# Kernel tuning notes

Hardware: AMD Instinct MI355X
Metric: run time of the kernel (lower is better)

The kernel has to match this reference:

```python
import jax, jax.numpy as jnp
import numpy as np

SEQ_LEN, BATCH, HID, ATT = 2048, 64, 512, 512


def setup_inputs() -> dict:
    key = jax.random.key(0)
    k1, k2, k3, k4, k5, k6 = jax.random.split(key, 6)
    return {
        "dec_out": jax.random.normal(k1, (BATCH, HID), dtype=jnp.float32),
        "enc_outs": jax.random.normal(k2, (SEQ_LEN, BATCH, HID), dtype=jnp.float32),
        "W_s": jax.random.normal(k3, (ATT, HID), dtype=jnp.float32) * (1.0 / np.sqrt(HID)),
        "W_t": jax.random.normal(k4, (ATT, HID), dtype=jnp.float32) * (1.0 / np.sqrt(HID)),
        "b_t": jax.random.normal(k5, (ATT,), dtype=jnp.float32) * 0.01,
        "v_a": jax.random.uniform(k6, (ATT,), dtype=jnp.float32, minval=-0.05, maxval=0.05),
    }


def reference(dec_out, enc_outs, W_s, W_t, b_t, v_a):
    # enc_att: (seq_len, batch, att) = W_s @ enc_outs
    enc_att = jnp.einsum('sbh,ah->sba', enc_outs, W_s)
    # dec_att: (batch, att) = W_t @ dec_out + b_t
    dec_att = dec_out @ W_t.T + b_t
    # score(b, s) = v_a . tanh(enc_att[s,b] + dec_att[b])
    scores = jnp.einsum('sba,a->bs', jnp.tanh(enc_att + dec_att[None, :, :]), v_a)
    return scores  # (batch, seq_len)
```

## Files before the change

kernel.cpp:

```cpp
#include <hip/hip_runtime.h>

typedef __attribute__((ext_vector_type(8))) short short8;
typedef __attribute__((ext_vector_type(4))) float f32x4;

#define SEQ 2048
#define BATCH 64
#define HID 512
#define ATT 512

__device__ __forceinline__ unsigned short f2bf(float f) {
  unsigned u = __float_as_uint(f);
  u += 0x7fffu + ((u >> 16) & 1u);
  return (unsigned short)(u >> 16);
}

__device__ __forceinline__ void dma16(const void* g, void* l) {
  __builtin_amdgcn_global_load_lds(
      (const __attribute__((address_space(1))) unsigned int*)g,
      (__attribute__((address_space(3))) unsigned int*)l, 16, 0, 0);
}

__device__ __forceinline__ short8 cvt8(float4 lo, float4 hi) {
  union { unsigned u[4]; short8 s; } r;
  asm("v_cvt_pk_bf16_f32 %0, %1, %2" : "=v"(r.u[0]) : "v"(lo.x), "v"(lo.y));
  asm("v_cvt_pk_bf16_f32 %0, %1, %2" : "=v"(r.u[1]) : "v"(lo.z), "v"(lo.w));
  asm("v_cvt_pk_bf16_f32 %0, %1, %2" : "=v"(r.u[2]) : "v"(hi.x), "v"(hi.y));
  asm("v_cvt_pk_bf16_f32 %0, %1, %2" : "=v"(r.u[3]) : "v"(hi.z), "v"(hi.w));
  return r.s;
}

#define GLOADS(dst, voff, base, OFF) \
  asm volatile("global_load_dwordx4 %0, %1, %2 offset:" #OFF \
               : "=v"(dst) : "v"(voff), "s"(base))

#define BWAIT(N, b0, b1, b2, b3) \
  asm volatile("s_waitcnt vmcnt(" #N ")" \
               : "+v"(b0), "+v"(b1), "+v"(b2), "+v"(b3) :: "memory")

__global__ void bahdanau_pre(const float* __restrict__ dec_out,
                             const float* __restrict__ W_t,
                             const float* __restrict__ b_t,
                             const float* __restrict__ W_s,
                             unsigned short* __restrict__ wsb,
                             float* __restrict__ decT) {
  if (blockIdx.x < 64) {
    const int b = blockIdx.x;
    __shared__ float drow[HID];
    for (int i = threadIdx.x; i < HID; i += 256) drow[i] = dec_out[b * HID + i];
    __syncthreads();
    for (int a = threadIdx.x; a < ATT; a += 256) {
      const float4* wr = (const float4*)(W_t + (size_t)a * HID);
      float s0 = 0.f, s1 = 0.f, s2 = 0.f, s3 = 0.f;
#pragma unroll 4
      for (int j = 0; j < HID / 4; ++j) {
        float4 w = wr[j];
        s0 = fmaf(w.x, drow[4 * j + 0], s0);
        s1 = fmaf(w.y, drow[4 * j + 1], s1);
        s2 = fmaf(w.z, drow[4 * j + 2], s2);
        s3 = fmaf(w.w, drow[4 * j + 3], s3);
      }
      decT[a * BATCH + b] = (s0 + s1) + (s2 + s3) + b_t[a];
    }
  } else {
    const int cb = blockIdx.x - 64;
    const float4* src = (const float4*)W_s;
#pragma unroll
    for (int i = 0; i < 4; ++i) {
      int idx = cb * 1024 + i * 256 + threadIdx.x;
      float4 v = src[idx];
      int a = idx >> 7;
      int h = (idx & 127) * 4;
      ushort4 o;
      o.x = f2bf(v.x); o.y = f2bf(v.y); o.z = f2bf(v.z); o.w = f2bf(v.w);
      int blk = (a >> 4) * 64 + ((h >> 3) & 3) * 16 + (a & 15);
      int dst = (h >> 5) * 16384 + blk * 8 + (h & 7);
      *(ushort4*)&wsb[dst] = o;
    }
  }
}

__global__ __launch_bounds__(512, 4)
void bahdanau_main(const float* __restrict__ enc,
                   const unsigned short* __restrict__ wsb,
                   const float* __restrict__ decT,
                   const float* __restrict__ v_a,
                   float* __restrict__ out) {
  __shared__ __align__(16) float Asm[4][2048];
  __shared__ float partial[512];

  const int tid  = threadIdx.x;
  const int w    = tid >> 6;
  const int lane = tid & 63;
  const int c = lane & 15;
  const int q = lane >> 4;
  const int s = blockIdx.x;
  const int n0 = w * 64;

  const char* encB = (const char*)(enc + (size_t)s * 64 * HID);

  const int am = (w & 3) * 16 + c;
  const int ag = q * 2 + (w >> 2);
  const char* aSrc = encB + am * 2048 + ag * 16;

  const unsigned voff = (unsigned)(w * 256 + q * 16 + c) * 16u;

  f32x4 acc[4][4];
#pragma unroll
  for (int nt = 0; nt < 4; ++nt)
#pragma unroll
    for (int mt = 0; mt < 4; ++mt)
      acc[mt][nt] = *(const f32x4*)(decT + (size_t)(n0 + nt * 16 + c) * 64 + mt * 16 + q * 4);

  asm volatile("s_waitcnt vmcnt(0)" ::: "memory");

  short8 bf[2][4];

  dma16(aSrc, &Asm[0][w * 256]);
  GLOADS(bf[0][0], voff, wsb, 0);
  GLOADS(bf[0][1], voff, wsb, 1024);
  GLOADS(bf[0][2], voff, wsb, 2048);
  GLOADS(bf[0][3], voff, wsb, 3072);
  dma16(aSrc + 128, &Asm[1][w * 256]);

#pragma unroll
  for (int kb = 0; kb < 16; ++kb) {
    if (kb + 1 < 16) {
      const unsigned short* bk = wsb + (size_t)(kb + 1) * 16384;
      GLOADS(bf[(kb + 1) & 1][0], voff, bk, 0);
      GLOADS(bf[(kb + 1) & 1][1], voff, bk, 1024);
      GLOADS(bf[(kb + 1) & 1][2], voff, bk, 2048);
      GLOADS(bf[(kb + 1) & 1][3], voff, bk, 3072);
    }
    if (kb + 2 < 16)
      dma16(aSrc + (kb + 2) * 128, &Asm[(kb + 2) & 3][w * 256]);

    if (kb <= 13)      BWAIT(6, bf[kb & 1][0], bf[kb & 1][1], bf[kb & 1][2], bf[kb & 1][3]);
    else if (kb == 14) BWAIT(5, bf[kb & 1][0], bf[kb & 1][1], bf[kb & 1][2], bf[kb & 1][3]);
    else               BWAIT(0, bf[kb & 1][0], bf[kb & 1][1], bf[kb & 1][2], bf[kb & 1][3]);
    __builtin_amdgcn_s_barrier();

    const float* Ac = &Asm[kb & 3][0];
#pragma unroll
    for (int mt = 0; mt < 4; ++mt) {
      float4 lo = *(const float4*)(Ac + (mt * 64 + q * 16 + c) * 4);
      float4 hi = *(const float4*)(Ac + (256 + mt * 64 + q * 16 + c) * 4);
      short8 af = cvt8(lo, hi);
#pragma unroll
      for (int nt = 0; nt < 4; ++nt)
        acc[mt][nt] = __builtin_amdgcn_mfma_f32_16x16x32_bf16(af, bf[kb & 1][nt], acc[mt][nt], 0, 0, 0);
    }
    asm volatile("s_waitcnt lgkmcnt(0)" ::: "memory");
  }

  float va[4];
#pragma unroll
  for (int nt = 0; nt < 4; ++nt) va[nt] = v_a[n0 + nt * 16 + c];

  float rowsum[4][4];
#pragma unroll
  for (int mt = 0; mt < 4; ++mt) {
#pragma unroll
    for (int r = 0; r < 4; ++r) {
      float sum = 0.f;
#pragma unroll
      for (int nt = 0; nt < 4; ++nt) {
        float x = acc[mt][nt][r];
        float e = __builtin_amdgcn_exp2f(x * 2.8853900817779268f);
        float t = 1.f - 2.f * __builtin_amdgcn_rcpf(e + 1.f);
        sum = fmaf(va[nt], t, sum);
      }
      rowsum[mt][r] = sum;
    }
  }

#pragma unroll
  for (int off = 1; off < 16; off <<= 1) {
#pragma unroll
    for (int mt = 0; mt < 4; ++mt)
#pragma unroll
      for (int r = 0; r < 4; ++r)
        rowsum[mt][r] += __shfl_xor(rowsum[mt][r], off, 64);
  }

  if (c == 0) {
#pragma unroll
    for (int mt = 0; mt < 4; ++mt)
#pragma unroll
      for (int r = 0; r < 4; ++r)
        partial[w * 64 + mt * 16 + q * 4 + r] = rowsum[mt][r];
  }
  __syncthreads();

  if (tid < 64) {
    float sum = 0.f;
#pragma unroll
    for (int ww = 0; ww < 8; ++ww) sum += partial[ww * 64 + tid];
    out[(size_t)tid * SEQ + s] = sum;
  }
}

extern "C" void kernel_launch(void* const* d_in, const int* in_sizes, int n_in,
                              void* d_out, int out_size, void* d_ws, size_t ws_size,
                              hipStream_t stream) {
  const float* dec_out = (const float*)d_in[0];
  const float* enc     = (const float*)d_in[1];
  const float* W_s     = (const float*)d_in[2];
  const float* W_t     = (const float*)d_in[3];
  const float* b_t     = (const float*)d_in[4];
  const float* v_a     = (const float*)d_in[5];
  float* out = (float*)d_out;

  unsigned short* wsb = (unsigned short*)d_ws;
  float* decT = (float*)((char*)d_ws + (size_t)ATT * HID * 2);

  bahdanau_pre<<<128, 256, 0, stream>>>(dec_out, W_t, b_t, W_s, wsb, decT);
  bahdanau_main<<<SEQ, 512, 0, stream>>>(enc, wsb, decT, v_a, out);
}
```

Baseline: 482.4 us.

## Deepen encoder LDS prefetch to 4 stages with XOR-swizzled layout

The LDS ring for encoder tiles grows from 4 to 8 slots, and the DMA prefetch distance grows from 2 to 4 k-blocks. The vmcnt waits are retuned to match the new pipeline depth. The LDS layout changes to row-major with an XOR swizzle, read through explicit ds_read_b128 with immediate offsets, to cut bank conflicts and address arithmetic. Doubling LDS per block drops the occupancy hint from 4 to 2 blocks per CU, trading latency hiding across blocks for deeper in-block prefetch.

```diff
diff --git a/kernel.cpp b/kernel.cpp
--- a/kernel.cpp
+++ b/kernel.cpp
@@ -36,6 +36,10 @@
 #define BWAIT(N, b0, b1, b2, b3) \
   asm volatile("s_waitcnt vmcnt(" #N ")" \
                : "+v"(b0), "+v"(b1), "+v"(b2), "+v"(b3) :: "memory")
+
+#define DSREAD(dst, vaddr, IMM) \
+  asm volatile("ds_read_b128 %0, %1 offset:%2" \
+               : "=v"(dst) : "v"(vaddr), "i"(IMM))
 
 __global__ void bahdanau_pre(const float* __restrict__ dec_out,
                              const float* __restrict__ W_t,
@@ -79,13 +83,13 @@
   }
 }
 
-__global__ __launch_bounds__(512, 4)
+__global__ __launch_bounds__(512, 2)
 void bahdanau_main(const float* __restrict__ enc,
                    const unsigned short* __restrict__ wsb,
                    const float* __restrict__ decT,
                    const float* __restrict__ v_a,
                    float* __restrict__ out) {
-  __shared__ __align__(16) float Asm[4][2048];
+  __shared__ __align__(16) float Asm[8][2048];
   __shared__ float partial[512];
 
   const int tid  = threadIdx.x;
@@ -93,16 +97,21 @@
   const int lane = tid & 63;
   const int c = lane & 15;
   const int q = lane >> 4;
+  const int x7 = c & 7;
   const int s = blockIdx.x;
   const int n0 = w * 64;
 
   const char* encB = (const char*)(enc + (size_t)s * 64 * HID);
 
-  const int am = (w & 3) * 16 + c;
-  const int ag = q * 2 + (w >> 2);
-  const char* aSrc = encB + am * 2048 + ag * 16;
+  const int am   = w * 8 + (lane >> 3);
+  const int jsrc = (lane & 7) ^ (lane >> 3);
+  const char* aSrc = encB + am * 2048 + jsrc * 16;
 
   const unsigned voff = (unsigned)(w * 256 + q * 16 + c) * 16u;
+
+  const unsigned lA = (unsigned)(size_t)(__attribute__((address_space(3))) char*)&Asm[0][0];
+  const unsigned loOff = lA + (unsigned)(c * 128 + (((2 * q)    ) ^ x7) * 16);
+  const unsigned hiOff = lA + (unsigned)(c * 128 + (((2 * q) | 1) ^ x7) * 16);
 
   f32x4 acc[4][4];
 #pragma unroll
@@ -115,12 +124,14 @@
 
   short8 bf[2][4];
 
-  dma16(aSrc, &Asm[0][w * 256]);
+  dma16(aSrc,       (char*)&Asm[0][0] + w * 1024);
+  dma16(aSrc + 128, (char*)&Asm[1][0] + w * 1024);
+  dma16(aSrc + 256, (char*)&Asm[2][0] + w * 1024);
+  dma16(aSrc + 384, (char*)&Asm[3][0] + w * 1024);
   GLOADS(bf[0][0], voff, wsb, 0);
   GLOADS(bf[0][1], voff, wsb, 1024);
   GLOADS(bf[0][2], voff, wsb, 2048);
   GLOADS(bf[0][3], voff, wsb, 3072);
-  dma16(aSrc + 128, &Asm[1][w * 256]);
 
 #pragma unroll
   for (int kb = 0; kb < 16; ++kb) {
@@ -131,25 +142,39 @@
       GLOADS(bf[(kb + 1) & 1][2], voff, bk, 2048);
       GLOADS(bf[(kb + 1) & 1][3], voff, bk, 3072);
     }
-    if (kb + 2 < 16)
-      dma16(aSrc + (kb + 2) * 128, &Asm[(kb + 2) & 3][w * 256]);
-
-    if (kb <= 13)      BWAIT(6, bf[kb & 1][0], bf[kb & 1][1], bf[kb & 1][2], bf[kb & 1][3]);
-    else if (kb == 14) BWAIT(5, bf[kb & 1][0], bf[kb & 1][1], bf[kb & 1][2], bf[kb & 1][3]);
+    if (kb + 4 < 16)
+      dma16(aSrc + (kb + 4) * 128, (char*)&Asm[(kb + 4) & 7][0] + w * 1024);
+
+    if (kb == 0)       BWAIT(5, bf[kb & 1][0], bf[kb & 1][1], bf[kb & 1][2], bf[kb & 1][3]);
+    else if (kb <= 11) BWAIT(6, bf[kb & 1][0], bf[kb & 1][1], bf[kb & 1][2], bf[kb & 1][3]);
+    else if (kb == 12) BWAIT(5, bf[kb & 1][0], bf[kb & 1][1], bf[kb & 1][2], bf[kb & 1][3]);
+    else if (kb <= 14) BWAIT(4, bf[kb & 1][0], bf[kb & 1][1], bf[kb & 1][2], bf[kb & 1][3]);
     else               BWAIT(0, bf[kb & 1][0], bf[kb & 1][1], bf[kb & 1][2], bf[kb & 1][3]);
     __builtin_amdgcn_s_barrier();
 
-    const float* Ac = &Asm[kb & 3][0];
-#pragma unroll
-    for (int mt = 0; mt < 4; ++mt) {
-      float4 lo = *(const float4*)(Ac + (mt * 64 + q * 16 + c) * 4);
-      float4 hi = *(const float4*)(Ac + (256 + mt * 64 + q * 16 + c) * 4);
-      short8 af = cvt8(lo, hi);
-#pragma unroll
-      for (int nt = 0; nt < 4; ++nt)
-        acc[mt][nt] = __builtin_amdgcn_mfma_f32_16x16x32_bf16(af, bf[kb & 1][nt], acc[mt][nt], 0, 0, 0);
-    }
+    float4 lo0, hi0, lo1, hi1, lo2, hi2, lo3, hi3;
+    DSREAD(lo0, loOff, ((kb & 7) * 8192 + 0 * 2048));
+    DSREAD(hi0, hiOff, ((kb & 7) * 8192 + 0 * 2048));
+    DSREAD(lo1, loOff, ((kb & 7) * 8192 + 1 * 2048));
+    DSREAD(hi1, hiOff, ((kb & 7) * 8192 + 1 * 2048));
+    DSREAD(lo2, loOff, ((kb & 7) * 8192 + 2 * 2048));
+    DSREAD(hi2, hiOff, ((kb & 7) * 8192 + 2 * 2048));
+    DSREAD(lo3, loOff, ((kb & 7) * 8192 + 3 * 2048));
+    DSREAD(hi3, hiOff, ((kb & 7) * 8192 + 3 * 2048));
     asm volatile("s_waitcnt lgkmcnt(0)" ::: "memory");
+    __builtin_amdgcn_sched_barrier(0);
+
+    short8 af0 = cvt8(lo0, hi0);
+    short8 af1 = cvt8(lo1, hi1);
+    short8 af2 = cvt8(lo2, hi2);
+    short8 af3 = cvt8(lo3, hi3);
+#pragma unroll
+    for (int nt = 0; nt < 4; ++nt) {
+      acc[0][nt] = __builtin_amdgcn_mfma_f32_16x16x32_bf16(af0, bf[kb & 1][nt], acc[0][nt], 0, 0, 0);
+      acc[1][nt] = __builtin_amdgcn_mfma_f32_16x16x32_bf16(af1, bf[kb & 1][nt], acc[1][nt], 0, 0, 0);
+      acc[2][nt] = __builtin_amdgcn_mfma_f32_16x16x32_bf16(af2, bf[kb & 1][nt], acc[2][nt], 0, 0, 0);
+      acc[3][nt] = __builtin_amdgcn_mfma_f32_16x16x32_bf16(af3, bf[kb & 1][nt], acc[3][nt], 0, 0, 0);
+    }
   }
 
   float va[4];
```

After: 469.1 us. 2.7% less time.
